# Performance work log

Measured on AMD Instinct MI355X. Metric: run time of the kernel, lower is better.

The kernel has to match this reference:

```python
import jax, jax.numpy as jnp
import numpy as np

N = 50000          # nodes
E = 800000         # directed edges (before self-loops)
IN_C = 512
HID = 256
HEADS = 8
HEAD_C = HID // HEADS
OUT_C = 64
NEG_SLOPE = 0.2    # PyG GATConv default LeakyReLU slope
EPS = 1e-16        # PyG softmax denominator epsilon


def _gat_layer(h, src, dst, a_src, a_dst):
    """One GATConv propagate step (eval mode, no attention dropout).
    h: [N, H, C] transformed node features; src/dst: [Etot] edge endpoints.
    Returns aggregated [N, H, C]."""
    # per-node attention logits: [N, H]
    alpha_src = jnp.einsum('nhc,hc->nh', h, a_src)
    alpha_dst = jnp.einsum('nhc,hc->nh', h, a_dst)
    e = alpha_src[src] + alpha_dst[dst]                      # [Etot, H]
    e = jnp.where(e > 0, e, NEG_SLOPE * e)                   # LeakyReLU
    # segment softmax over incoming edges of each dst node
    e_max = jax.ops.segment_max(e, dst, num_segments=N)      # [N, H]
    e_exp = jnp.exp(e - e_max[dst])                          # [Etot, H]
    denom = jax.ops.segment_sum(e_exp, dst, num_segments=N)  # [N, H]
    alpha = e_exp / (denom[dst] + EPS)                       # [Etot, H]
    msg = alpha[:, :, None] * h[src]                         # [Etot, H, C]
    return jax.ops.segment_sum(msg, dst, num_segments=N)     # [N, H, C]


def setup_inputs() -> dict:
    key = jax.random.key(0)
    ks = jax.random.split(key, 10)
    s1 = 1.0 / np.sqrt(IN_C)
    s2 = 1.0 / np.sqrt(HID)
    return {
        'x': jax.random.normal(ks[0], (N, IN_C), jnp.float32),
        'edge_index': jax.random.randint(ks[1], (2, E), 0, N, dtype=jnp.int64),
        'W1': jax.random.normal(ks[2], (IN_C, HID), jnp.float32) * s1,
        'a_src1': jax.random.normal(ks[3], (HEADS, HEAD_C), jnp.float32) * 0.1,
        'a_dst1': jax.random.normal(ks[4], (HEADS, HEAD_C), jnp.float32) * 0.1,
        'b1': jnp.zeros((HID,), jnp.float32),
        'W2': jax.random.normal(ks[5], (HID, OUT_C), jnp.float32) * s2,
        'a_src2': jax.random.normal(ks[6], (1, OUT_C), jnp.float32) * 0.1,
        'a_dst2': jax.random.normal(ks[7], (1, OUT_C), jnp.float32) * 0.1,
        'b2': jnp.zeros((OUT_C,), jnp.float32),
    }


def reference(x, edge_index, W1, a_src1, a_dst1, b1, W2, a_src2, a_dst2, b2):
    # PyG GATConv: add self-loops (default add_self_loops=True)
    loops = jnp.arange(N, dtype=edge_index.dtype)
    src = jnp.concatenate([edge_index[0], loops])
    dst = jnp.concatenate([edge_index[1], loops])

    # conv1: heads=8, concat=True
    h1 = (x @ W1).reshape(N, HEADS, HEAD_C)
    h1 = _gat_layer(h1, src, dst, a_src1, a_dst1).reshape(N, HID) + b1
    h1 = jax.nn.elu(h1)

    # conv2: heads=1, concat=False (mean over 1 head == identity)
    h2 = (h1 @ W2).reshape(N, 1, OUT_C)
    out = _gat_layer(h2, src, dst, a_src2, a_dst2).mean(axis=1) + b2
    return out
```

## Files before the change

### kernel.cpp

```cpp
#include <hip/hip_runtime.h>

#define N_NODES 50000
#define M_PAD   50048
#define NBLK    196
#define E_EDGES 800000
#define E_TOT   (E_EDGES + N_NODES)
#define IN_C 512
#define HID 256
#define HEADS 8
#define OUT_C 64

#define MM1_BLOCKS (M_PAD / 128)
#define SCAT_BLOCKS ((E_TOT + 511) / 512)
#define CNT_BLOCKS  ((E_TOT + 511) / 512)
#define CONVW_ELEMS (HID * IN_C + OUT_C * HID)
#define CONVW_BLOCKS ((CONVW_ELEMS + 511) / 512)

typedef unsigned int uint;
typedef unsigned short ushort_t;
typedef __bf16 bf16x8 __attribute__((ext_vector_type(8)));
typedef float f32x4 __attribute__((ext_vector_type(4)));
typedef float f32x2 __attribute__((ext_vector_type(2)));

__device__ __forceinline__ float lrelu(float x) { return x > 0.f ? x : 0.2f * x; }

__device__ __forceinline__ unsigned short f2bf(float f) {
  __bf16 b = (__bf16)f;
  return __builtin_bit_cast(unsigned short, b);
}
__device__ __forceinline__ float bflo(uint u) { return __uint_as_float(u << 16); }
__device__ __forceinline__ float bfhi(uint u) { return __uint_as_float(u & 0xFFFF0000u); }
__device__ __forceinline__ f32x2 unp2(uint u) {
  f32x2 r; r.x = bflo(u); r.y = bfhi(u); return r;
}

__global__ __launch_bounds__(512) void k_fatA(const int* __restrict__ ei,
                                              int* __restrict__ counts,
                                              const float* __restrict__ W1,
                                              const float* __restrict__ W2,
                                              ushort_t* __restrict__ w1t,
                                              ushort_t* __restrict__ w2t) {
  int bid = blockIdx.x;
  if (bid < CNT_BLOCKS) {
    int e = bid * 512 + threadIdx.x;
    if (e >= E_TOT) return;
    int d = (e < E_EDGES) ? ei[E_EDGES + e] : (e - E_EDGES);
    atomicAdd(&counts[d], 1);
  } else {
    int t = (bid - CNT_BLOCKS) * 512 + threadIdx.x;
    if (t < HID * IN_C) {
      int n = t >> 9, k = t & 511;
      w1t[t] = f2bf(W1[(size_t)k * HID + n]);
    } else if (t < CONVW_ELEMS) {
      int u = t - HID * IN_C;
      int n = u >> 8, k = u & 255;
      w2t[u] = f2bf(W2[(size_t)k * OUT_C + n]);
    }
  }
}

__global__ void k_bsum(const int* __restrict__ counts, int* __restrict__ bsum) {
  int i = blockIdx.x * 256 + threadIdx.x;
  int v = (i < N_NODES) ? counts[i] : 0;
  __shared__ int ws[4];
  int lane = threadIdx.x & 63, wid = threadIdx.x >> 6;
  #pragma unroll
  for (int off = 32; off; off >>= 1) v += __shfl_xor(v, off);
  if (lane == 0) ws[wid] = v;
  __syncthreads();
  if (threadIdx.x == 0) bsum[blockIdx.x] = ws[0] + ws[1] + ws[2] + ws[3];
}

__global__ void k_bscan(const int* __restrict__ bsum, int* __restrict__ boff) {
  int tid = threadIdx.x;
  int v = (tid < NBLK) ? bsum[tid] : 0;
  int lane = tid & 63, wid = tid >> 6;
  int x = v;
  #pragma unroll
  for (int off = 1; off < 64; off <<= 1) {
    int t = __shfl_up(x, off);
    if (lane >= off) x += t;
  }
  __shared__ int ws[4];
  if (lane == 63) ws[wid] = x;
  __syncthreads();
  int woff = 0;
  for (int w = 0; w < wid; w++) woff += ws[w];
  if (tid < NBLK) boff[tid] = x + woff - v;
}

__global__ void k_local(const int* __restrict__ counts, const int* __restrict__ boff,
                        int* __restrict__ indptr, int* __restrict__ wptr) {
  int b = blockIdx.x;
  int i = b * 256 + threadIdx.x;
  int v = (i < N_NODES) ? counts[i] : 0;
  int lane = threadIdx.x & 63, wid = threadIdx.x >> 6;
  int x = v;
  #pragma unroll
  for (int off = 1; off < 64; off <<= 1) {
    int t = __shfl_up(x, off);
    if (lane >= off) x += t;
  }
  __shared__ int ws[4];
  if (lane == 63) ws[wid] = x;
  __syncthreads();
  int woff = boff[b];
  for (int w = 0; w < wid; w++) woff += ws[w];
  int excl = woff + x - v;
  if (i < N_NODES) { indptr[i] = excl; wptr[i] = excl; }
  if (b == 0 && threadIdx.x == 0) indptr[N_NODES] = E_TOT;
}

__global__ __launch_bounds__(512) void k_fatB(const float* __restrict__ A,
                                              const ushort_t* __restrict__ Bt,
                                              const float* __restrict__ asrc1,
                                              const float* __restrict__ adst1,
                                              ushort_t* __restrict__ Cb,
                                              float* __restrict__ as1,
                                              float* __restrict__ ad1,
                                              const int* __restrict__ ei,
                                              int* __restrict__ wptr,
                                              int* __restrict__ csr_src) {
  if (blockIdx.x >= MM1_BLOCKS) {
    int e = (blockIdx.x - MM1_BLOCKS) * 512 + threadIdx.x;
    if (e >= E_TOT) return;
    int s, d;
    if (e < E_EDGES) { s = ei[e]; d = ei[E_EDGES + e]; }
    else { s = d = e - E_EDGES; }
    int pos = atomicAdd(&wptr[d], 1);
    csr_src[pos] = s;
    return;
  }
  __shared__ ushort_t sA[128][40];
  __shared__ ushort_t sB[256][40];
  int tid = threadIdx.x;
  int wid = tid >> 6, lane = tid & 63;
  int wm = wid >> 2, wn = wid & 3;
  int lr = lane & 15, kg = lane >> 4;
  int row0 = blockIdx.x * 128;
  f32x4 acc[4][4] = {};

  for (int k0 = 0; k0 < IN_C; k0 += 32) {
    {
      int r = tid >> 2, cs = (tid & 3) * 8;
      int gr = row0 + r;
      unsigned short v[8];
      if (gr < N_NODES) {
        const float* src = A + (size_t)gr * IN_C + k0 + cs;
        float4 f0 = *reinterpret_cast<const float4*>(src);
        float4 f1 = *reinterpret_cast<const float4*>(src + 4);
        v[0] = f2bf(f0.x); v[1] = f2bf(f0.y); v[2] = f2bf(f0.z); v[3] = f2bf(f0.w);
        v[4] = f2bf(f1.x); v[5] = f2bf(f1.y); v[6] = f2bf(f1.z); v[7] = f2bf(f1.w);
      } else {
        #pragma unroll
        for (int i = 0; i < 8; i++) v[i] = 0;
      }
      uint4 pk;
      pk.x = v[0] | ((uint)v[1] << 16); pk.y = v[2] | ((uint)v[3] << 16);
      pk.z = v[4] | ((uint)v[5] << 16); pk.w = v[6] | ((uint)v[7] << 16);
      *reinterpret_cast<uint4*>(&sA[r][cs]) = pk;
    }
    {
      int n = tid >> 1, ks = (tid & 1) * 16;
      const ushort_t* src = Bt + (size_t)n * IN_C + k0 + ks;
      uint4 v0 = *reinterpret_cast<const uint4*>(src);
      uint4 v1 = *reinterpret_cast<const uint4*>(src + 8);
      *reinterpret_cast<uint4*>(&sB[n][ks]) = v0;
      *reinterpret_cast<uint4*>(&sB[n][ks + 8]) = v1;
    }
    __syncthreads();

    bf16x8 af[4], bfr[4];
    #pragma unroll
    for (int i = 0; i < 4; i++)
      af[i] = *reinterpret_cast<const bf16x8*>(&sA[wm * 64 + i * 16 + lr][kg * 8]);
    #pragma unroll
    for (int j = 0; j < 4; j++)
      bfr[j] = *reinterpret_cast<const bf16x8*>(&sB[wn * 64 + j * 16 + lr][kg * 8]);
    #pragma unroll
    for (int i = 0; i < 4; i++)
      #pragma unroll
      for (int j = 0; j < 4; j++)
        acc[i][j] = __builtin_amdgcn_mfma_f32_16x16x32_bf16(af[i], bfr[j], acc[i][j], 0, 0, 0);
    __syncthreads();
  }

  {
    int h0 = wn * 2, h1 = wn * 2 + 1;
    float a0s = asrc1[h0 * 32 + lr], a1s = asrc1[h0 * 32 + 16 + lr];
    float a2s = asrc1[h1 * 32 + lr], a3s = asrc1[h1 * 32 + 16 + lr];
    float a0d = adst1[h0 * 32 + lr], a1d = adst1[h0 * 32 + 16 + lr];
    float a2d = adst1[h1 * 32 + lr], a3d = adst1[h1 * 32 + 16 + lr];
    #pragma unroll
    for (int i = 0; i < 4; i++) {
      #pragma unroll
      for (int q = 0; q < 4; q++) {
        float s0 = acc[i][0][q] * a0s + acc[i][1][q] * a1s;
        float s1 = acc[i][2][q] * a2s + acc[i][3][q] * a3s;
        float d0 = acc[i][0][q] * a0d + acc[i][1][q] * a1d;
        float d1 = acc[i][2][q] * a2d + acc[i][3][q] * a3d;
        #pragma unroll
        for (int off = 1; off < 16; off <<= 1) {
          s0 += __shfl_xor(s0, off);
          s1 += __shfl_xor(s1, off);
          d0 += __shfl_xor(d0, off);
          d1 += __shfl_xor(d1, off);
        }
        int gr = row0 + wm * 64 + i * 16 + kg * 4 + q;
        if (lr == 0 && gr < N_NODES) {
          as1[gr * 8 + h0] = s0;
          as1[gr * 8 + h1] = s1;
          ad1[gr * 8 + h0] = d0;
          ad1[gr * 8 + h1] = d1;
        }
      }
    }
  }

  #pragma unroll
  for (int i = 0; i < 4; i++) {
    #pragma unroll
    for (int j = 0; j < 4; j++) {
      int gc = wn * 64 + j * 16 + lr;
      #pragma unroll
      for (int q = 0; q < 4; q++) {
        int gr = row0 + wm * 64 + i * 16 + kg * 4 + q;
        if (gr < N_NODES) Cb[(size_t)gr * HID + gc] = f2bf(acc[i][j][q]);
      }
    }
  }
}

__global__ __launch_bounds__(256) void k_mm2(const ushort_t* __restrict__ At,
                                             const ushort_t* __restrict__ Bt,
                                             const float* __restrict__ asrc2,
                                             const float* __restrict__ adst2,
                                             ushort_t* __restrict__ Cb,
                                             float* __restrict__ as2,
                                             float* __restrict__ ad2) {
  __shared__ ushort_t sA[128][40];
  __shared__ ushort_t sB[64][40];
  int tid = threadIdx.x;
  int wid = tid >> 6, lane = tid & 63;
  int lr = lane & 15, kg = lane >> 4;
  int row0 = blockIdx.x * 128;
  f32x4 acc[2][4] = {};

  for (int kt = 0; kt < HID / 32; ++kt) {
    {
      const ushort_t* src = At + ((size_t)blockIdx.x * 8 + kt) * 4096 + tid * 16;
      uint4 v0 = *reinterpret_cast<const uint4*>(src);
      uint4 v1 = *reinterpret_cast<const uint4*>(src + 8);
      int r = tid >> 1, ks = (tid & 1) * 16;
      *reinterpret_cast<uint4*>(&sA[r][ks]) = v0;
      *reinterpret_cast<uint4*>(&sA[r][ks + 8]) = v1;
    }
    if (tid < 128) {
      int n = tid >> 1, ks = (tid & 1) * 16;
      const ushort_t* src = Bt + (size_t)n * HID + kt * 32 + ks;
      uint4 v0 = *reinterpret_cast<const uint4*>(src);
      uint4 v1 = *reinterpret_cast<const uint4*>(src + 8);
      *reinterpret_cast<uint4*>(&sB[n][ks]) = v0;
      *reinterpret_cast<uint4*>(&sB[n][ks + 8]) = v1;
    }
    __syncthreads();

    bf16x8 af[2], bfr[4];
    #pragma unroll
    for (int i = 0; i < 2; i++)
      af[i] = *reinterpret_cast<const bf16x8*>(&sA[wid * 32 + i * 16 + lr][kg * 8]);
    #pragma unroll
    for (int j = 0; j < 4; j++)
      bfr[j] = *reinterpret_cast<const bf16x8*>(&sB[j * 16 + lr][kg * 8]);
    #pragma unroll
    for (int i = 0; i < 2; i++)
      #pragma unroll
      for (int j = 0; j < 4; j++)
        acc[i][j] = __builtin_amdgcn_mfma_f32_16x16x32_bf16(af[i], bfr[j], acc[i][j], 0, 0, 0);
    __syncthreads();
  }

  {
    float avs[4], avd[4];
    #pragma unroll
    for (int j = 0; j < 4; j++) {
      avs[j] = asrc2[j * 16 + lr];
      avd[j] = adst2[j * 16 + lr];
    }
    #pragma unroll
    for (int i = 0; i < 2; i++) {
      #pragma unroll
      for (int q = 0; q < 4; q++) {
        float s = acc[i][0][q] * avs[0] + acc[i][1][q] * avs[1]
                + acc[i][2][q] * avs[2] + acc[i][3][q] * avs[3];
        float d = acc[i][0][q] * avd[0] + acc[i][1][q] * avd[1]
                + acc[i][2][q] * avd[2] + acc[i][3][q] * avd[3];
        #pragma unroll
        for (int off = 1; off < 16; off <<= 1) {
          s += __shfl_xor(s, off);
          d += __shfl_xor(d, off);
        }
        int gr = row0 + wid * 32 + i * 16 + kg * 4 + q;
        if (lr == 0 && gr < N_NODES) { as2[gr] = s; ad2[gr] = d; }
      }
    }
  }

  #pragma unroll
  for (int i = 0; i < 2; i++) {
    #pragma unroll
    for (int j = 0; j < 4; j++) {
      int gc = j * 16 + lr;
      #pragma unroll
      for (int q = 0; q < 4; q++) {
        int gr = row0 + wid * 32 + i * 16 + kg * 4 + q;
        if (gr < N_NODES) Cb[(size_t)gr * OUT_C + gc] = f2bf(acc[i][j][q]);
      }
    }
  }
}

__global__ __launch_bounds__(256) void k_agg1(const ushort_t* __restrict__ h1b,
                                              const int* __restrict__ indptr,
                                              const int* __restrict__ csr_src,
                                              const float* __restrict__ as1,
                                              const float* __restrict__ ad1,
                                              const float* __restrict__ b1,
                                              ushort_t* __restrict__ hpb) {
  int wave = threadIdx.x >> 6, lane = threadIdx.x & 63;
  int node = blockIdx.x * 4 + wave;
  if (node >= N_NODES) return;
  int beg = indptr[node], end = indptr[node + 1];
  int half = lane >> 5, sl = lane & 31, h = sl >> 2;
  float adst = ad1[node * 8 + h];

  f32x2 a0 = {0.f, 0.f}, a1 = {0.f, 0.f}, a2 = {0.f, 0.f}, a3 = {0.f, 0.f};
  float dsum = 0.f;
  int e = beg + half;
  for (; e + 6 < end; e += 8) {
    int s0 = csr_src[e];
    int s1 = csr_src[e + 2];
    int s2 = csr_src[e + 4];
    int s3 = csr_src[e + 6];
    float l0 = as1[s0 * 8 + h];
    float l1 = as1[s1 * 8 + h];
    float l2 = as1[s2 * 8 + h];
    float l3 = as1[s3 * 8 + h];
    uint4 r0 = *reinterpret_cast<const uint4*>(&h1b[(size_t)s0 * HID + sl * 8]);
    uint4 r1 = *reinterpret_cast<const uint4*>(&h1b[(size_t)s1 * HID + sl * 8]);
    uint4 r2 = *reinterpret_cast<const uint4*>(&h1b[(size_t)s2 * HID + sl * 8]);
    uint4 r3 = *reinterpret_cast<const uint4*>(&h1b[(size_t)s3 * HID + sl * 8]);
    float w0 = __expf(lrelu(l0 + adst));
    float w1 = __expf(lrelu(l1 + adst));
    float w2 = __expf(lrelu(l2 + adst));
    float w3 = __expf(lrelu(l3 + adst));
    a0 += w0 * unp2(r0.x); a1 += w0 * unp2(r0.y); a2 += w0 * unp2(r0.z); a3 += w0 * unp2(r0.w);
    a0 += w1 * unp2(r1.x); a1 += w1 * unp2(r1.y); a2 += w1 * unp2(r1.z); a3 += w1 * unp2(r1.w);
    a0 += w2 * unp2(r2.x); a1 += w2 * unp2(r2.y); a2 += w2 * unp2(r2.z); a3 += w2 * unp2(r2.w);
    a0 += w3 * unp2(r3.x); a1 += w3 * unp2(r3.y); a2 += w3 * unp2(r3.z); a3 += w3 * unp2(r3.w);
    dsum += w0 + w1 + w2 + w3;
  }
  for (; e < end; e += 2) {
    int s = csr_src[e];
    float w = __expf(lrelu(as1[s * 8 + h] + adst));
    uint4 rv = *reinterpret_cast<const uint4*>(&h1b[(size_t)s * HID + sl * 8]);
    a0 += w * unp2(rv.x); a1 += w * unp2(rv.y); a2 += w * unp2(rv.z); a3 += w * unp2(rv.w);
    dsum += w;
  }
  float acc[8] = {a0.x, a0.y, a1.x, a1.y, a2.x, a2.y, a3.x, a3.y};
  #pragma unroll
  for (int j = 0; j < 8; j++) acc[j] += __shfl_xor(acc[j], 32);
  dsum += __shfl_xor(dsum, 32);
  float inv = 1.f / (dsum + 1e-16f);

  if (half == 0) {
    unsigned short ob[8];
    #pragma unroll
    for (int j = 0; j < 8; j++) {
      float o = acc[j] * inv + b1[sl * 8 + j];
      o = o > 0.f ? o : expm1f(o);
      ob[j] = f2bf(o);
    }
    uint4 pk;
    pk.x = ob[0] | ((uint)ob[1] << 16); pk.y = ob[2] | ((uint)ob[3] << 16);
    pk.z = ob[4] | ((uint)ob[5] << 16); pk.w = ob[6] | ((uint)ob[7] << 16);
    size_t addr = ((size_t)(node >> 7) * 8 + (sl >> 2)) * 4096 + (size_t)(node & 127) * 32 + (sl & 3) * 8;
    *reinterpret_cast<uint4*>(&hpb[addr]) = pk;
  }
}

__global__ __launch_bounds__(256) void k_agg2(const ushort_t* __restrict__ h2b,
                                              const int* __restrict__ indptr,
                                              const int* __restrict__ csr_src,
                                              const float* __restrict__ as2,
                                              const float* __restrict__ ad2,
                                              const float* __restrict__ b2,
                                              float* __restrict__ out) {
  int wave = threadIdx.x >> 6, lane = threadIdx.x & 63;
  int node = blockIdx.x * 4 + wave;
  if (node >= N_NODES) return;
  int beg = indptr[node], end = indptr[node + 1];
  int half = lane >> 5, sl = lane & 31;
  float adst = ad2[node];

  f32x2 acc2 = {0.f, 0.f};
  float dsum = 0.f;
  int e = beg + half;
  for (; e + 6 < end; e += 8) {
    int s0 = csr_src[e];
    int s1 = csr_src[e + 2];
    int s2 = csr_src[e + 4];
    int s3 = csr_src[e + 6];
    float l0 = as2[s0];
    float l1 = as2[s1];
    float l2 = as2[s2];
    float l3 = as2[s3];
    uint v0 = *reinterpret_cast<const uint*>(&h2b[(size_t)s0 * OUT_C + sl * 2]);
    uint v1 = *reinterpret_cast<const uint*>(&h2b[(size_t)s1 * OUT_C + sl * 2]);
    uint v2 = *reinterpret_cast<const uint*>(&h2b[(size_t)s2 * OUT_C + sl * 2]);
    uint v3 = *reinterpret_cast<const uint*>(&h2b[(size_t)s3 * OUT_C + sl * 2]);
    float w0 = __expf(lrelu(l0 + adst));
    float w1 = __expf(lrelu(l1 + adst));
    float w2 = __expf(lrelu(l2 + adst));
    float w3 = __expf(lrelu(l3 + adst));
    acc2 += w0 * unp2(v0); acc2 += w1 * unp2(v1);
    acc2 += w2 * unp2(v2); acc2 += w3 * unp2(v3);
    dsum += w0 + w1 + w2 + w3;
  }
  for (; e < end; e += 2) {
    int s = csr_src[e];
    float w = __expf(lrelu(as2[s] + adst));
    uint v = *reinterpret_cast<const uint*>(&h2b[(size_t)s * OUT_C + sl * 2]);
    acc2 += w * unp2(v);
    dsum += w;
  }
  acc2.x += __shfl_xor(acc2.x, 32);
  acc2.y += __shfl_xor(acc2.y, 32);
  dsum += __shfl_xor(dsum, 32);
  float inv = 1.f / (dsum + 1e-16f);
  if (half == 0) {
    float2 o = {acc2.x * inv + b2[sl * 2], acc2.y * inv + b2[sl * 2 + 1]};
    *reinterpret_cast<float2*>(&out[(size_t)node * OUT_C + sl * 2]) = o;
  }
}

extern "C" void kernel_launch(void* const* d_in, const int* in_sizes, int n_in,
                              void* d_out, int out_size, void* d_ws, size_t ws_size,
                              hipStream_t stream) {
  const float* x     = (const float*)d_in[0];
  const int*   ei    = (const int*)d_in[1];
  const float* W1    = (const float*)d_in[2];
  const float* asrc1 = (const float*)d_in[3];
  const float* adst1 = (const float*)d_in[4];
  const float* b1    = (const float*)d_in[5];
  const float* W2    = (const float*)d_in[6];
  const float* asrc2 = (const float*)d_in[7];
  const float* adst2 = (const float*)d_in[8];
  const float* b2    = (const float*)d_in[9];
  float* out = (float*)d_out;

  char* p = (char*)d_ws;
  size_t off = 0;
  auto take = [&](size_t bytes) -> void* {
    void* r = p + off;
    off += (bytes + 255) & ~(size_t)255;
    return r;
  };
  ushort_t* h1b  = (ushort_t*)take((size_t)N_NODES * HID * 2);
  ushort_t* hpb  = (ushort_t*)take((size_t)(M_PAD / 128) * 8 * 4096 * 2);
  ushort_t* h2b  = (ushort_t*)take((size_t)N_NODES * OUT_C * 2);
  float*    as1  = (float*)take((size_t)N_NODES * HEADS * 4);
  float*    ad1  = (float*)take((size_t)N_NODES * HEADS * 4);
  float*    as2  = (float*)take((size_t)N_NODES * 4);
  float*    ad2  = (float*)take((size_t)N_NODES * 4);
  int* counts = (int*)take((size_t)N_NODES * 4);
  int* indptr = (int*)take((size_t)(N_NODES + 1) * 4);
  int* wptr   = (int*)take((size_t)(N_NODES + 1) * 4);
  int* bsum   = (int*)take((size_t)NBLK * 4);
  int* boff   = (int*)take((size_t)NBLK * 4);
  int* csr    = (int*)take((size_t)E_TOT * 4);
  ushort_t* w1t = (ushort_t*)take((size_t)IN_C * HID * 2);
  ushort_t* w2t = (ushort_t*)take((size_t)HID * OUT_C * 2);

  hipMemsetAsync(counts, 0, (size_t)N_NODES * 4, stream);
  k_fatA<<<CNT_BLOCKS + CONVW_BLOCKS, 512, 0, stream>>>(ei, counts, W1, W2, w1t, w2t);
  k_bsum<<<NBLK, 256, 0, stream>>>(counts, bsum);
  k_bscan<<<1, 256, 0, stream>>>(bsum, boff);
  k_local<<<NBLK, 256, 0, stream>>>(counts, boff, indptr, wptr);

  k_fatB<<<MM1_BLOCKS + SCAT_BLOCKS, 512, 0, stream>>>(x, w1t, asrc1, adst1, h1b, as1, ad1,
                                                       ei, wptr, csr);

  k_agg1<<<(N_NODES + 3) / 4, 256, 0, stream>>>(h1b, indptr, csr, as1, ad1, b1, hpb);

  k_mm2<<<M_PAD / 128, 256, 0, stream>>>(hpb, w2t, asrc2, adst2, h2b, as2, ad2);
  k_agg2<<<(N_NODES + 3) / 4, 256, 0, stream>>>(h2b, indptr, csr, as2, ad2, b2, out);
}
```

Baseline: 240.8 us.

## Split layer-1 GEMM tiles across column halves with 256-thread blocks

Changes the fused GEMM+scatter kernel from 512-thread blocks covering 128x256 output tiles to 256-thread blocks covering 128x128 tiles, with two column blocks per row tile. It also halves the scatter block size. This doubles the number of GEMM blocks for better CU occupancy and load balance on the fused launch, at the cost of reading and converting the fp32 x tile twice, once per column half.

```diff
diff --git a/kernel.cpp b/kernel.cpp
--- a/kernel.cpp
+++ b/kernel.cpp
@@ -10,8 +10,9 @@
 #define HEADS 8
 #define OUT_C 64
 
-#define MM1_BLOCKS (M_PAD / 128)
-#define SCAT_BLOCKS ((E_TOT + 511) / 512)
+#define MM1_BX 391
+#define MM1_BLK (MM1_BX * 2)
+#define SCAT_BLOCKS ((E_TOT + 255) / 256)
 #define CNT_BLOCKS  ((E_TOT + 511) / 512)
 #define CONVW_ELEMS (HID * IN_C + OUT_C * HID)
 #define CONVW_BLOCKS ((CONVW_ELEMS + 511) / 512)
@@ -111,7 +112,7 @@
   if (b == 0 && threadIdx.x == 0) indptr[N_NODES] = E_TOT;
 }
 
-__global__ __launch_bounds__(512) void k_fatB(const float* __restrict__ A,
+__global__ __launch_bounds__(256) void k_fatB(const float* __restrict__ A,
                                               const ushort_t* __restrict__ Bt,
                                               const float* __restrict__ asrc1,
                                               const float* __restrict__ adst1,
@@ -121,8 +122,8 @@
                                               const int* __restrict__ ei,
                                               int* __restrict__ wptr,
                                               int* __restrict__ csr_src) {
-  if (blockIdx.x >= MM1_BLOCKS) {
-    int e = (blockIdx.x - MM1_BLOCKS) * 512 + threadIdx.x;
+  if (blockIdx.x >= MM1_BLK) {
+    int e = (blockIdx.x - MM1_BLK) * 256 + threadIdx.x;
     if (e >= E_TOT) return;
     int s, d;
     if (e < E_EDGES) { s = ei[e]; d = ei[E_EDGES + e]; }
@@ -131,38 +132,45 @@
     csr_src[pos] = s;
     return;
   }
+  int bx = blockIdx.x >> 1, by = blockIdx.x & 1;
   __shared__ ushort_t sA[128][40];
-  __shared__ ushort_t sB[256][40];
+  __shared__ ushort_t sB[128][40];
   int tid = threadIdx.x;
   int wid = tid >> 6, lane = tid & 63;
-  int wm = wid >> 2, wn = wid & 3;
+  int wm = wid >> 1, wn = wid & 1;
   int lr = lane & 15, kg = lane >> 4;
-  int row0 = blockIdx.x * 128;
+  int row0 = bx * 128;
+  int cb0 = by * 128;
   f32x4 acc[4][4] = {};
 
   for (int k0 = 0; k0 < IN_C; k0 += 32) {
     {
-      int r = tid >> 2, cs = (tid & 3) * 8;
+      int r = tid >> 1, cs = (tid & 1) * 16;
       int gr = row0 + r;
-      unsigned short v[8];
+      unsigned short v[16];
       if (gr < N_NODES) {
         const float* src = A + (size_t)gr * IN_C + k0 + cs;
-        float4 f0 = *reinterpret_cast<const float4*>(src);
-        float4 f1 = *reinterpret_cast<const float4*>(src + 4);
-        v[0] = f2bf(f0.x); v[1] = f2bf(f0.y); v[2] = f2bf(f0.z); v[3] = f2bf(f0.w);
-        v[4] = f2bf(f1.x); v[5] = f2bf(f1.y); v[6] = f2bf(f1.z); v[7] = f2bf(f1.w);
+        #pragma unroll
+        for (int i = 0; i < 4; i++) {
+          float4 f = *reinterpret_cast<const float4*>(src + i * 4);
+          v[i * 4 + 0] = f2bf(f.x); v[i * 4 + 1] = f2bf(f.y);
+          v[i * 4 + 2] = f2bf(f.z); v[i * 4 + 3] = f2bf(f.w);
+        }
       } else {
         #pragma unroll
-        for (int i = 0; i < 8; i++) v[i] = 0;
+        for (int i = 0; i < 16; i++) v[i] = 0;
       }
-      uint4 pk;
-      pk.x = v[0] | ((uint)v[1] << 16); pk.y = v[2] | ((uint)v[3] << 16);
-      pk.z = v[4] | ((uint)v[5] << 16); pk.w = v[6] | ((uint)v[7] << 16);
-      *reinterpret_cast<uint4*>(&sA[r][cs]) = pk;
+      uint4 p0, p1;
+      p0.x = v[0] | ((uint)v[1] << 16);  p0.y = v[2] | ((uint)v[3] << 16);
+      p0.z = v[4] | ((uint)v[5] << 16);  p0.w = v[6] | ((uint)v[7] << 16);
+      p1.x = v[8] | ((uint)v[9] << 16);  p1.y = v[10] | ((uint)v[11] << 16);
+      p1.z = v[12] | ((uint)v[13] << 16); p1.w = v[14] | ((uint)v[15] << 16);
+      *reinterpret_cast<uint4*>(&sA[r][cs]) = p0;
+      *reinterpret_cast<uint4*>(&sA[r][cs + 8]) = p1;
     }
     {
       int n = tid >> 1, ks = (tid & 1) * 16;
-      const ushort_t* src = Bt + (size_t)n * IN_C + k0 + ks;
+      const ushort_t* src = Bt + (size_t)(cb0 + n) * IN_C + k0 + ks;
       uint4 v0 = *reinterpret_cast<const uint4*>(src);
       uint4 v1 = *reinterpret_cast<const uint4*>(src + 8);
       *reinterpret_cast<uint4*>(&sB[n][ks]) = v0;
@@ -186,7 +194,7 @@
   }
 
   {
-    int h0 = wn * 2, h1 = wn * 2 + 1;
+    int h0 = by * 4 + wn * 2, h1 = h0 + 1;
     float a0s = asrc1[h0 * 32 + lr], a1s = asrc1[h0 * 32 + 16 + lr];
     float a2s = asrc1[h1 * 32 + lr], a3s = asrc1[h1 * 32 + 16 + lr];
     float a0d = adst1[h0 * 32 + lr], a1d = adst1[h0 * 32 + 16 + lr];
@@ -221,7 +229,7 @@
   for (int i = 0; i < 4; i++) {
     #pragma unroll
     for (int j = 0; j < 4; j++) {
-      int gc = wn * 64 + j * 16 + lr;
+      int gc = cb0 + wn * 64 + j * 16 + lr;
       #pragma unroll
       for (int q = 0; q < 4; q++) {
         int gr = row0 + wm * 64 + i * 16 + kg * 4 + q;
@@ -488,8 +496,8 @@
   k_bscan<<<1, 256, 0, stream>>>(bsum, boff);
   k_local<<<NBLK, 256, 0, stream>>>(counts, boff, indptr, wptr);
 
-  k_fatB<<<MM1_BLOCKS + SCAT_BLOCKS, 512, 0, stream>>>(x, w1t, asrc1, adst1, h1b, as1, ad1,
-                                                       ei, wptr, csr);
+  k_fatB<<<MM1_BLK + SCAT_BLOCKS, 256, 0, stream>>>(x, w1t, asrc1, adst1, h1b, as1, ad1,
+                                                    ei, wptr, csr);
 
   k_agg1<<<(N_NODES + 3) / 4, 256, 0, stream>>>(h1b, indptr, csr, as1, ad1, b1, hpb);
 
```

Result: no change. 238.7 us (median of 2 runs) (-0.9%).

## Drop LDS staging in layer-1 GEMM; each wave computes 16 rows by all columns

Applied to the files above, without the earlier changes.

The fused first-layer GEMM no longer stages A and B tiles through shared memory with block barriers. Each wave now owns 16 rows across all 256 output columns. It loads its A fragment straight from global memory, converting fp32 to bf16 in registers, and reads the B fragments directly from global memory, relying on the caches. The attention logits for all 8 heads are reduced inside one wave. This removes the LDS writes, LDS reads and __syncthreads, but every wave now re-reads the whole W1 from cache instead of sharing it across the block, so cache bandwidth pressure rises.

```diff
diff --git a/kernel.cpp b/kernel.cpp
--- a/kernel.cpp
+++ b/kernel.cpp
@@ -10,8 +10,8 @@
 #define HEADS 8
 #define OUT_C 64
 
-#define MM1_BLOCKS (M_PAD / 128)
-#define SCAT_BLOCKS ((E_TOT + 511) / 512)
+#define MM1B 391
+#define SCATB ((E_TOT + 511) / 512)
 #define CNT_BLOCKS  ((E_TOT + 511) / 512)
 #define CONVW_ELEMS (HID * IN_C + OUT_C * HID)
 #define CONVW_BLOCKS ((CONVW_ELEMS + 511) / 512)
@@ -121,8 +121,8 @@
                                               const int* __restrict__ ei,
                                               int* __restrict__ wptr,
                                               int* __restrict__ csr_src) {
-  if (blockIdx.x >= MM1_BLOCKS) {
-    int e = (blockIdx.x - MM1_BLOCKS) * 512 + threadIdx.x;
+  if (blockIdx.x >= MM1B) {
+    int e = (blockIdx.x - MM1B) * 512 + threadIdx.x;
     if (e >= E_TOT) return;
     int s, d;
     if (e < E_EDGES) { s = ei[e]; d = ei[E_EDGES + e]; }
@@ -131,102 +131,72 @@
     csr_src[pos] = s;
     return;
   }
-  __shared__ ushort_t sA[128][40];
-  __shared__ ushort_t sB[256][40];
   int tid = threadIdx.x;
-  int wid = tid >> 6, lane = tid & 63;
-  int wm = wid >> 2, wn = wid & 3;
+  int w = tid >> 6, lane = tid & 63;
   int lr = lane & 15, kg = lane >> 4;
-  int row0 = blockIdx.x * 128;
-  f32x4 acc[4][4] = {};
-
+  int grow = blockIdx.x * 128 + w * 16;
+  int arow = grow + lr;
+  bool valid = arow < N_NODES;
+  const float* ax = A + (size_t)(valid ? arow : 0) * IN_C + kg * 8;
+
+  f32x4 acc[16] = {};
+
+  #pragma unroll 2
   for (int k0 = 0; k0 < IN_C; k0 += 32) {
-    {
-      int r = tid >> 2, cs = (tid & 3) * 8;
-      int gr = row0 + r;
-      unsigned short v[8];
-      if (gr < N_NODES) {
-        const float* src = A + (size_t)gr * IN_C + k0 + cs;
-        float4 f0 = *reinterpret_cast<const float4*>(src);
-        float4 f1 = *reinterpret_cast<const float4*>(src + 4);
-        v[0] = f2bf(f0.x); v[1] = f2bf(f0.y); v[2] = f2bf(f0.z); v[3] = f2bf(f0.w);
-        v[4] = f2bf(f1.x); v[5] = f2bf(f1.y); v[6] = f2bf(f1.z); v[7] = f2bf(f1.w);
-      } else {
-        #pragma unroll
-        for (int i = 0; i < 8; i++) v[i] = 0;
+    float4 fa0, fa1;
+    if (valid) {
+      fa0 = *reinterpret_cast<const float4*>(ax + k0);
+      fa1 = *reinterpret_cast<const float4*>(ax + k0 + 4);
+    } else {
+      fa0 = make_float4(0.f, 0.f, 0.f, 0.f);
+      fa1 = make_float4(0.f, 0.f, 0.f, 0.f);
+    }
+    bf16x8 af;
+    af[0] = (__bf16)fa0.x; af[1] = (__bf16)fa0.y;
+    af[2] = (__bf16)fa0.z; af[3] = (__bf16)fa0.w;
+    af[4] = (__bf16)fa1.x; af[5] = (__bf16)fa1.y;
+    af[6] = (__bf16)fa1.z; af[7] = (__bf16)fa1.w;
+
+    const ushort_t* bp = Bt + k0 + kg * 8 + (size_t)lr * IN_C;
+    #pragma unroll
+    for (int j = 0; j < 16; j++) {
+      bf16x8 bfr = *reinterpret_cast<const bf16x8*>(bp + (size_t)j * 16 * IN_C);
+      acc[j] = __builtin_amdgcn_mfma_f32_16x16x32_bf16(af, bfr, acc[j], 0, 0, 0);
+    }
+  }
+
+  #pragma unroll
+  for (int q = 0; q < 4; q++) {
+    int gr = grow + kg * 4 + q;
+    float sv[8], dv[8];
+    #pragma unroll
+    for (int h = 0; h < 8; h++) {
+      float a0s = asrc1[h * 32 + lr], a1s = asrc1[h * 32 + 16 + lr];
+      float a0d = adst1[h * 32 + lr], a1d = adst1[h * 32 + 16 + lr];
+      float s = acc[2 * h][q] * a0s + acc[2 * h + 1][q] * a1s;
+      float d = acc[2 * h][q] * a0d + acc[2 * h + 1][q] * a1d;
+      #pragma unroll
+      for (int off = 1; off < 16; off <<= 1) {
+        s += __shfl_xor(s, off);
+        d += __shfl_xor(d, off);
       }
-      uint4 pk;
-      pk.x = v[0] | ((uint)v[1] << 16); pk.y = v[2] | ((uint)v[3] << 16);
-      pk.z = v[4] | ((uint)v[5] << 16); pk.w = v[6] | ((uint)v[7] << 16);
-      *reinterpret_cast<uint4*>(&sA[r][cs]) = pk;
-    }
-    {
-      int n = tid >> 1, ks = (tid & 1) * 16;
-      const ushort_t* src = Bt + (size_t)n * IN_C + k0 + ks;
-      uint4 v0 = *reinterpret_cast<const uint4*>(src);
-      uint4 v1 = *reinterpret_cast<const uint4*>(src + 8);
-      *reinterpret_cast<uint4*>(&sB[n][ks]) = v0;
-      *reinterpret_cast<uint4*>(&sB[n][ks + 8]) = v1;
-    }
-    __syncthreads();
-
-    bf16x8 af[4], bfr[4];
-    #pragma unroll
-    for (int i = 0; i < 4; i++)
-      af[i] = *reinterpret_cast<const bf16x8*>(&sA[wm * 64 + i * 16 + lr][kg * 8]);
-    #pragma unroll
-    for (int j = 0; j < 4; j++)
-      bfr[j] = *reinterpret_cast<const bf16x8*>(&sB[wn * 64 + j * 16 + lr][kg * 8]);
-    #pragma unroll
-    for (int i = 0; i < 4; i++)
+      sv[h] = s; dv[h] = d;
+    }
+    if (lr == 0 && gr < N_NODES) {
       #pragma unroll
-      for (int j = 0; j < 4; j++)
-        acc[i][j] = __builtin_amdgcn_mfma_f32_16x16x32_bf16(af[i], bfr[j], acc[i][j], 0, 0, 0);
-    __syncthreads();
-  }
-
-  {
-    int h0 = wn * 2, h1 = wn * 2 + 1;
-    float a0s = asrc1[h0 * 32 + lr], a1s = asrc1[h0 * 32 + 16 + lr];
-    float a2s = asrc1[h1 * 32 + lr], a3s = asrc1[h1 * 32 + 16 + lr];
-    float a0d = adst1[h0 * 32 + lr], a1d = adst1[h0 * 32 + 16 + lr];
-    float a2d = adst1[h1 * 32 + lr], a3d = adst1[h1 * 32 + 16 + lr];
-    #pragma unroll
-    for (int i = 0; i < 4; i++) {
-      #pragma unroll
-      for (int q = 0; q < 4; q++) {
-        float s0 = acc[i][0][q] * a0s + acc[i][1][q] * a1s;
-        float s1 = acc[i][2][q] * a2s + acc[i][3][q] * a3s;
-        float d0 = acc[i][0][q] * a0d + acc[i][1][q] * a1d;
-        float d1 = acc[i][2][q] * a2d + acc[i][3][q] * a3d;
-        #pragma unroll
-        for (int off = 1; off < 16; off <<= 1) {
-          s0 += __shfl_xor(s0, off);
-          s1 += __shfl_xor(s1, off);
-          d0 += __shfl_xor(d0, off);
-          d1 += __shfl_xor(d1, off);
-        }
-        int gr = row0 + wm * 64 + i * 16 + kg * 4 + q;
-        if (lr == 0 && gr < N_NODES) {
-          as1[gr * 8 + h0] = s0;
-          as1[gr * 8 + h1] = s1;
-          ad1[gr * 8 + h0] = d0;
-          ad1[gr * 8 + h1] = d1;
-        }
+      for (int h = 0; h < 8; h++) {
+        as1[gr * 8 + h] = sv[h];
+        ad1[gr * 8 + h] = dv[h];
       }
     }
   }
 
   #pragma unroll
-  for (int i = 0; i < 4; i++) {
-    #pragma unroll
-    for (int j = 0; j < 4; j++) {
-      int gc = wn * 64 + j * 16 + lr;
-      #pragma unroll
-      for (int q = 0; q < 4; q++) {
-        int gr = row0 + wm * 64 + i * 16 + kg * 4 + q;
-        if (gr < N_NODES) Cb[(size_t)gr * HID + gc] = f2bf(acc[i][j][q]);
-      }
+  for (int j = 0; j < 16; j++) {
+    #pragma unroll
+    for (int q = 0; q < 4; q++) {
+      int gr = grow + kg * 4 + q;
+      if (gr < N_NODES) Cb[(size_t)gr * HID + j * 16 + lr] = f2bf(acc[j][q]);
     }
   }
 }
@@ -488,8 +458,8 @@
   k_bscan<<<1, 256, 0, stream>>>(bsum, boff);
   k_local<<<NBLK, 256, 0, stream>>>(counts, boff, indptr, wptr);
 
-  k_fatB<<<MM1_BLOCKS + SCAT_BLOCKS, 512, 0, stream>>>(x, w1t, asrc1, adst1, h1b, as1, ad1,
-                                                       ei, wptr, csr);
+  k_fatB<<<MM1B + SCATB, 512, 0, stream>>>(x, w1t, asrc1, adst1, h1b, as1, ad1,
+                                           ei, wptr, csr);
 
   k_agg1<<<(N_NODES + 3) / 4, 256, 0, stream>>>(h1b, indptr, csr, as1, ad1, b1, hpb);
 
```

Result: slower. 306.0 us (+27.1%).

## Pre-convert x to tiled bf16 and split GEMM1 into two column blocks

Applied to the files above, without the earlier changes.

Converts x from fp32 to bf16 in a separate pass inside the first fused kernel, writing it in a tiled 128x32 layout so the GEMM's A-tile loads become contiguous 16-byte reads. GEMM1 is also split into two 128-column halves per row tile with 256-thread blocks, which doubles the block count and lowers per-block LDS use. The aim is to halve the fp32 read traffic inside the GEMM and raise occupancy. The cost is an extra full read and write of x plus a 51MB scratch buffer, and each bf16 x tile is now read twice, once per column half.

```diff
diff --git a/kernel.cpp b/kernel.cpp
--- a/kernel.cpp
+++ b/kernel.cpp
@@ -10,11 +10,13 @@
 #define HEADS 8
 #define OUT_C 64
 
-#define MM1_BLOCKS (M_PAD / 128)
-#define SCAT_BLOCKS ((E_TOT + 511) / 512)
+#define MM1_BX 391
+#define MM1_BLK (MM1_BX * 2)
+#define SCAT_BLOCKS ((E_TOT + 255) / 256)
 #define CNT_BLOCKS  ((E_TOT + 511) / 512)
 #define CONVW_ELEMS (HID * IN_C + OUT_C * HID)
 #define CONVW_BLOCKS ((CONVW_ELEMS + 511) / 512)
+#define CONVX_BLOCKS (M_PAD * 64 / 512)
 
 typedef unsigned int uint;
 typedef unsigned short ushort_t;
@@ -38,15 +40,17 @@
                                               int* __restrict__ counts,
                                               const float* __restrict__ W1,
                                               const float* __restrict__ W2,
+                                              const float* __restrict__ x,
                                               ushort_t* __restrict__ w1t,
-                                              ushort_t* __restrict__ w2t) {
+                                              ushort_t* __restrict__ w2t,
+                                              ushort_t* __restrict__ xb) {
   int bid = blockIdx.x;
   if (bid < CNT_BLOCKS) {
     int e = bid * 512 + threadIdx.x;
     if (e >= E_TOT) return;
     int d = (e < E_EDGES) ? ei[E_EDGES + e] : (e - E_EDGES);
     atomicAdd(&counts[d], 1);
-  } else {
+  } else if (bid < CNT_BLOCKS + CONVW_BLOCKS) {
     int t = (bid - CNT_BLOCKS) * 512 + threadIdx.x;
     if (t < HID * IN_C) {
       int n = t >> 9, k = t & 511;
@@ -56,6 +60,26 @@
       int n = u >> 8, k = u & 255;
       w2t[u] = f2bf(W2[(size_t)k * OUT_C + n]);
     }
+  } else {
+    int t = (bid - CNT_BLOCKS - CONVW_BLOCKS) * 512 + threadIdx.x;
+    int r = t >> 6, c8 = t & 63;
+    if (r >= M_PAD) return;
+    unsigned short v[8];
+    if (r < N_NODES) {
+      const float* src = x + (size_t)r * IN_C + c8 * 8;
+      float4 f0 = *reinterpret_cast<const float4*>(src);
+      float4 f1 = *reinterpret_cast<const float4*>(src + 4);
+      v[0] = f2bf(f0.x); v[1] = f2bf(f0.y); v[2] = f2bf(f0.z); v[3] = f2bf(f0.w);
+      v[4] = f2bf(f1.x); v[5] = f2bf(f1.y); v[6] = f2bf(f1.z); v[7] = f2bf(f1.w);
+    } else {
+      #pragma unroll
+      for (int i = 0; i < 8; i++) v[i] = 0;
+    }
+    size_t addr = ((size_t)(r >> 7) * 16 + (c8 >> 2)) * 4096 + ((r & 127) << 5) + ((c8 & 3) << 3);
+    uint4 pk;
+    pk.x = v[0] | ((uint)v[1] << 16); pk.y = v[2] | ((uint)v[3] << 16);
+    pk.z = v[4] | ((uint)v[5] << 16); pk.w = v[6] | ((uint)v[7] << 16);
+    *reinterpret_cast<uint4*>(xb + addr) = pk;
   }
 }
 
@@ -111,7 +135,7 @@
   if (b == 0 && threadIdx.x == 0) indptr[N_NODES] = E_TOT;
 }
 
-__global__ __launch_bounds__(512) void k_fatB(const float* __restrict__ A,
+__global__ __launch_bounds__(256) void k_fatB(const ushort_t* __restrict__ Ax,
                                               const ushort_t* __restrict__ Bt,
                                               const float* __restrict__ asrc1,
                                               const float* __restrict__ adst1,
@@ -121,8 +145,8 @@
                                               const int* __restrict__ ei,
                                               int* __restrict__ wptr,
                                               int* __restrict__ csr_src) {
-  if (blockIdx.x >= MM1_BLOCKS) {
-    int e = (blockIdx.x - MM1_BLOCKS) * 512 + threadIdx.x;
+  if (blockIdx.x >= MM1_BLK) {
+    int e = (blockIdx.x - MM1_BLK) * 256 + threadIdx.x;
     if (e >= E_TOT) return;
     int s, d;
     if (e < E_EDGES) { s = ei[e]; d = ei[E_EDGES + e]; }
@@ -131,38 +155,29 @@
     csr_src[pos] = s;
     return;
   }
+  int bx = blockIdx.x >> 1, by = blockIdx.x & 1;
   __shared__ ushort_t sA[128][40];
-  __shared__ ushort_t sB[256][40];
+  __shared__ ushort_t sB[128][40];
   int tid = threadIdx.x;
   int wid = tid >> 6, lane = tid & 63;
-  int wm = wid >> 2, wn = wid & 3;
+  int wm = wid >> 1, wn = wid & 1;
   int lr = lane & 15, kg = lane >> 4;
-  int row0 = blockIdx.x * 128;
+  int row0 = bx * 128;
+  int cb0 = by * 128;
   f32x4 acc[4][4] = {};
 
-  for (int k0 = 0; k0 < IN_C; k0 += 32) {
+  for (int kt = 0; kt < IN_C / 32; ++kt) {
     {
-      int r = tid >> 2, cs = (tid & 3) * 8;
-      int gr = row0 + r;
-      unsigned short v[8];
-      if (gr < N_NODES) {
-        const float* src = A + (size_t)gr * IN_C + k0 + cs;
-        float4 f0 = *reinterpret_cast<const float4*>(src);
-        float4 f1 = *reinterpret_cast<const float4*>(src + 4);
-        v[0] = f2bf(f0.x); v[1] = f2bf(f0.y); v[2] = f2bf(f0.z); v[3] = f2bf(f0.w);
-        v[4] = f2bf(f1.x); v[5] = f2bf(f1.y); v[6] = f2bf(f1.z); v[7] = f2bf(f1.w);
-      } else {
-        #pragma unroll
-        for (int i = 0; i < 8; i++) v[i] = 0;
-      }
-      uint4 pk;
-      pk.x = v[0] | ((uint)v[1] << 16); pk.y = v[2] | ((uint)v[3] << 16);
-      pk.z = v[4] | ((uint)v[5] << 16); pk.w = v[6] | ((uint)v[7] << 16);
-      *reinterpret_cast<uint4*>(&sA[r][cs]) = pk;
+      const ushort_t* src = Ax + ((size_t)bx * 16 + kt) * 4096 + tid * 16;
+      uint4 v0 = *reinterpret_cast<const uint4*>(src);
+      uint4 v1 = *reinterpret_cast<const uint4*>(src + 8);
+      int r = tid >> 1, ks = (tid & 1) * 16;
+      *reinterpret_cast<uint4*>(&sA[r][ks]) = v0;
+      *reinterpret_cast<uint4*>(&sA[r][ks + 8]) = v1;
     }
     {
       int n = tid >> 1, ks = (tid & 1) * 16;
-      const ushort_t* src = Bt + (size_t)n * IN_C + k0 + ks;
+      const ushort_t* src = Bt + (size_t)(cb0 + n) * IN_C + kt * 32 + ks;
       uint4 v0 = *reinterpret_cast<const uint4*>(src);
       uint4 v1 = *reinterpret_cast<const uint4*>(src + 8);
       *reinterpret_cast<uint4*>(&sB[n][ks]) = v0;
@@ -186,7 +201,7 @@
   }
 
   {
-    int h0 = wn * 2, h1 = wn * 2 + 1;
+    int h0 = by * 4 + wn * 2, h1 = h0 + 1;
     float a0s = asrc1[h0 * 32 + lr], a1s = asrc1[h0 * 32 + 16 + lr];
     float a2s = asrc1[h1 * 32 + lr], a3s = asrc1[h1 * 32 + 16 + lr];
     float a0d = adst1[h0 * 32 + lr], a1d = adst1[h0 * 32 + 16 + lr];
@@ -221,7 +236,7 @@
   for (int i = 0; i < 4; i++) {
     #pragma unroll
     for (int j = 0; j < 4; j++) {
-      int gc = wn * 64 + j * 16 + lr;
+      int gc = cb0 + wn * 64 + j * 16 + lr;
       #pragma unroll
       for (int q = 0; q < 4; q++) {
         int gr = row0 + wm * 64 + i * 16 + kg * 4 + q;
@@ -481,15 +496,17 @@
   int* csr    = (int*)take((size_t)E_TOT * 4);
   ushort_t* w1t = (ushort_t*)take((size_t)IN_C * HID * 2);
   ushort_t* w2t = (ushort_t*)take((size_t)HID * OUT_C * 2);
+  ushort_t* xb  = (ushort_t*)take((size_t)M_PAD * IN_C * 2);
 
   hipMemsetAsync(counts, 0, (size_t)N_NODES * 4, stream);
-  k_fatA<<<CNT_BLOCKS + CONVW_BLOCKS, 512, 0, stream>>>(ei, counts, W1, W2, w1t, w2t);
+  k_fatA<<<CNT_BLOCKS + CONVW_BLOCKS + CONVX_BLOCKS, 512, 0, stream>>>(
+      ei, counts, W1, W2, x, w1t, w2t, xb);
   k_bsum<<<NBLK, 256, 0, stream>>>(counts, bsum);
   k_bscan<<<1, 256, 0, stream>>>(bsum, boff);
   k_local<<<NBLK, 256, 0, stream>>>(counts, boff, indptr, wptr);
 
-  k_fatB<<<MM1_BLOCKS + SCAT_BLOCKS, 512, 0, stream>>>(x, w1t, asrc1, adst1, h1b, as1, ad1,
-                                                       ei, wptr, csr);
+  k_fatB<<<MM1_BLK + SCAT_BLOCKS, 256, 0, stream>>>(xb, w1t, asrc1, adst1, h1b, as1, ad1,
+                                                    ei, wptr, csr);
 
   k_agg1<<<(N_NODES + 3) / 4, 256, 0, stream>>>(h1b, indptr, csr, as1, ad1, b1, hpb);
 
```

Result: slower. 251.6 us (+4.5%).
